# Optimization experiments

Hardware: AMD Instinct MI355X
Metric: run time of the kernel (lower is better)

Reference implementation:

```python
import jax, jax.numpy as jnp
import numpy as np

IMG = 512
STRIDES = (8.0, 16.0, 32.0)   # p3, p4, p5
ROI = 7                        # roi_size
SR = 2                         # roi_align sampling ratio (fixed; torchvision default -1 is adaptive)
IOU_LOW, IOU_HIGH = 0.4, 0.6   # fg/bg matching thresholds (2nd-stage)
NUM_CLASSES = 20
B, R, M, C = 4, 256, 40, 256


def _make_boxes(key, b, n, max_wh):
    k1, k2 = jax.random.split(key)
    cxy = jax.random.uniform(k1, (b, n, 2), minval=0.0, maxval=float(IMG))
    wh = jax.random.uniform(k2, (b, n, 2), minval=16.0, maxval=float(max_wh))
    x1y1 = jnp.clip(cxy - wh / 2, 0.0, IMG - 1.0)
    x2y2 = jnp.clip(cxy + wh / 2, x1y1 + 1.0, float(IMG))
    return jnp.concatenate([x1y1, x2y2], axis=-1)


def setup_inputs() -> dict:
    key = jax.random.key(0)
    ks = jax.random.split(key, 12)
    feats_p3 = jax.random.normal(ks[0], (B, C, 64, 64), jnp.float32)
    feats_p4 = jax.random.normal(ks[1], (B, C, 32, 32), jnp.float32)
    feats_p5 = jax.random.normal(ks[2], (B, C, 16, 16), jnp.float32)
    props_p3 = _make_boxes(ks[3], B, R, 128)
    props_p4 = _make_boxes(ks[4], B, R, 256)
    props_p5 = _make_boxes(ks[5], B, R, 512)
    gt_xyxy = _make_boxes(ks[6], B, M, 400)
    gt_cls = jax.random.randint(ks[7], (B, M, 1), 0, NUM_CLASSES).astype(jnp.float32)
    gt = jnp.concatenate([gt_xyxy, gt_cls], axis=-1)
    pad = (jnp.arange(M) >= 25)[None, :, None]   # last 15 rows are padding (class -1)
    gt_boxes = jnp.where(pad, -1.0, gt)
    conv_w = jax.random.normal(ks[8], (C, C, 3, 3), jnp.float32) * 0.01
    conv_b = jnp.zeros((C,), jnp.float32)
    fc_w = jax.random.normal(ks[9], (NUM_CLASSES + 1, C * ROI * ROI), jnp.float32) * 0.01
    fc_b = jnp.zeros((NUM_CLASSES + 1,), jnp.float32)
    return {"feats_p3": feats_p3, "feats_p4": feats_p4, "feats_p5": feats_p5,
            "props_p3": props_p3, "props_p4": props_p4, "props_p5": props_p5,
            "gt_boxes": gt_boxes, "conv_w": conv_w, "conv_b": conv_b,
            "fc_w": fc_w, "fc_b": fc_b}


def _bilinear(feat, ys, xs):
    # feat: (C,H,W); ys: (R,G,1); xs: (R,1,G) -> (C,R,G,G)
    Cc, H, W = feat.shape
    valid = (ys >= -1.0) & (ys <= H) & (xs >= -1.0) & (xs <= W)
    y = jnp.clip(ys, 0.0, H - 1.0)
    x = jnp.clip(xs, 0.0, W - 1.0)
    y0f = jnp.floor(y); x0f = jnp.floor(x)
    y0 = y0f.astype(jnp.int32); x0 = x0f.astype(jnp.int32)
    y1 = jnp.minimum(y0 + 1, H - 1); x1 = jnp.minimum(x0 + 1, W - 1)
    ly = y - y0f; lx = x - x0f
    hy = 1.0 - ly; hx = 1.0 - lx
    v = (feat[:, y0, x0] * (hy * hx) + feat[:, y0, x1] * (hy * lx)
         + feat[:, y1, x0] * (ly * hx) + feat[:, y1, x1] * (ly * lx))
    return jnp.where(valid, v, 0.0)


def _roi_align(feat, rois, scale):
    # feat: (C,H,W); rois: (R,4) xyxy in image coords; aligned=True
    r = rois.shape[0]
    x1 = rois[:, 0] * scale - 0.5
    y1 = rois[:, 1] * scale - 0.5
    roi_w = rois[:, 2] * scale - 0.5 - x1
    roi_h = rois[:, 3] * scale - 0.5 - y1
    G = ROI * SR
    frac = (jnp.arange(G, dtype=feat.dtype) + 0.5) / G
    xs = x1[:, None] + frac[None, :] * roi_w[:, None]   # (R,G)
    ys = y1[:, None] + frac[None, :] * roi_h[:, None]
    v = _bilinear(feat, ys[:, :, None], xs[:, None, :])  # (C,R,G,G)
    v = v.transpose(1, 0, 2, 3).reshape(r, -1, ROI, SR, ROI, SR)
    return v.mean(axis=(3, 5))                            # (R,C,7,7)


def _iou(b1, b2):
    # b1: (N,4), b2: (M,4) -> (N,M)
    tl = jnp.maximum(b1[:, None, :2], b2[None, :, :2])
    br = jnp.minimum(b1[:, None, 2:4], b2[None, :, 2:4])
    inter = jnp.clip(br - tl, 0.0).prod(-1)
    a1 = (b1[:, 2:4] - b1[:, :2]).prod(-1)
    a2 = (b2[:, 2:4] - b2[:, :2]).prod(-1)
    return inter / (a1[:, None] + a2[None, :] - inter)


def _match(props, gt):
    # props: (N,4); gt: (M,5) padded with class -1
    valid = gt[:, 4] != -1
    m = jnp.where(valid[None, :], _iou(props, gt[:, :4]), -1.0)
    q = m.max(axis=1)
    matched = gt[m.argmax(axis=1)]                       # (N,5)
    matched = jnp.where((q <= IOU_LOW)[:, None], -1.0, matched)      # background
    matched = jnp.where(((q > IOU_LOW) & (q < IOU_HIGH))[:, None], -1e8, matched)  # neutral
    return matched


def reference(feats_p3, feats_p4, feats_p5, props_p3, props_p4, props_p5,
              gt_boxes, conv_w, conv_b, fc_w, fc_b):
    levels = [(feats_p3, props_p3, STRIDES[0]),
              (feats_p4, props_p4, STRIDES[1]),
              (feats_p5, props_p5, STRIDES[2])]
    # ROI-align every proposal at its level; order: image-major, then level, then roi
    per_level = [jax.vmap(lambda f, p, s=s: _roi_align(f, p, 1.0 / s))(f, p)
                 for f, p, s in levels]                   # each (B,R,C,7,7)
    roi_feats = jnp.stack(per_level, axis=1).reshape(-1, C, ROI, ROI)
    # cls head: conv3x3 + relu + flatten + linear
    h = jax.lax.conv_general_dilated(roi_feats, conv_w, (1, 1), 'SAME')
    h = jax.nn.relu(h + conv_b[None, :, None, None])
    logits = h.reshape(h.shape[0], -1) @ fc_w.T + fc_b    # (B*3*R, num_classes+1)
    # match concatenated per-image proposals to GT (no-grad pipeline)
    props_all = jnp.concatenate([props_p3, props_p4, props_p5], axis=1)  # (B,3R,4)
    matched = jax.vmap(_match)(jax.lax.stop_gradient(props_all), gt_boxes)
    return logits, matched
```

## Files before the change

### kernel.cpp

```cpp
#include <hip/hip_runtime.h>

typedef unsigned short ushort_t;
typedef __attribute__((ext_vector_type(4))) unsigned short ushort4_t;
typedef __attribute__((ext_vector_type(8))) short short8;
typedef __attribute__((ext_vector_type(4))) unsigned int uint4v;
typedef __attribute__((ext_vector_type(2))) float float2v;
typedef __attribute__((ext_vector_type(4))) float floatx4;
typedef __attribute__((ext_vector_type(16))) float floatx16;

#define B_ 4
#define C_ 256
#define R_ 256
#define M_ 40
#define NCLS 21
#define ROI_ 7
#define G_ 14
#define NROI_TOT 3072
#define PROPS_PER_IMG 768
#define POOL_PITCH 264
#define POOL_ROWS 148
#define WCONV_ELEMS (256 * 2304)
#define NKB 392
#define WFC2_ELEMS (NKB * 32 * 32)
#define OFF_FWB   WCONV_ELEMS
#define OFF_CL3   (OFF_FWB + WFC2_ELEMS)
#define OFF_CL4   (OFF_CL3 + 4 * 64 * 64 * 256)
#define OFF_CL5   (OFF_CL4 + 4 * 32 * 32 * 256)

__device__ __forceinline__ ushort_t f2bf(float f) {
  unsigned u = __builtin_bit_cast(unsigned, f);
  u += 0x7fff + ((u >> 16) & 1);
  return (ushort_t)(u >> 16);
}
__device__ __forceinline__ float2v cvt2(unsigned u) {
  float2v r;
  r[0] = __builtin_bit_cast(float, u << 16);
  r[1] = __builtin_bit_cast(float, u & 0xffff0000u);
  return r;
}

template <int W>
__device__ __forceinline__ void transpose_feat(const float* __restrict__ in,
                                               ushort_t* __restrict__ outp,
                                               const int fid, const int t,
                                               ushort_t* __restrict__ tile) {
  const int b = fid / W;
  const int y = fid - b * W;
  const float* src = in + (size_t)(b * 256) * (W * W) + (size_t)y * W;
#pragma unroll
  for (int i = 0; i < W / 4; ++i) {
    const int f4 = t + i * 256;
    const int c = f4 / (W / 4);
    const int x = (f4 - c * (W / 4)) * 4;
    const floatx4 v = *(const floatx4*)(src + (size_t)c * (W * W) + x);
    tile[c * 65 + x + 0] = f2bf(v[0]);
    tile[c * 65 + x + 1] = f2bf(v[1]);
    tile[c * 65 + x + 2] = f2bf(v[2]);
    tile[c * 65 + x + 3] = f2bf(v[3]);
  }
  __syncthreads();
  ushort_t* orow = outp + ((size_t)(b * W + y) * W) * 256;
#pragma unroll
  for (int i = 0; i < W / 4; ++i) {
    const int idx = t + i * 256;
    const int x = idx >> 6;
    const int c4 = (idx & 63) * 4;
    ushort4_t v;
    v[0] = tile[(c4 + 0) * 65 + x];
    v[1] = tile[(c4 + 1) * 65 + x];
    v[2] = tile[(c4 + 2) * 65 + x];
    v[3] = tile[(c4 + 3) * 65 + x];
    *(ushort4_t*)(orow + (size_t)x * 256 + c4) = v;
  }
}

__global__ __launch_bounds__(256) void prep_kernel(
    const float* __restrict__ cw, const float* __restrict__ fw,
    const float* __restrict__ f3, const float* __restrict__ f4,
    const float* __restrict__ f5, const float* __restrict__ p3,
    const float* __restrict__ p4, const float* __restrict__ p5,
    const float* __restrict__ gt, ushort_t* __restrict__ wr,
    ushort_t* __restrict__ fwb, ushort_t* __restrict__ cl3,
    ushort_t* __restrict__ cl4, ushort_t* __restrict__ cl5,
    float* __restrict__ out) {
  __shared__ ushort_t tile[256 * 65];
  const int id = blockIdx.x;
  const int t = threadIdx.x;

  if (id < 512) {
    const int i0 = id * 256 + t;
    const int stride = 512 * 256;
    for (int idx = i0; idx < WCONV_ELEMS; idx += stride) {
      const int kk = idx >> 12;
      const int rem = idx & 4095;
      const int co = rem >> 4;
      const int i = rem & 15;
      const int k = kk * 16 + i;
      const int j = k >> 8;
      const int ci = k & 255;
      wr[idx] = f2bf(cw[(co * 256 + ci) * 9 + j]);
    }
    for (int idx = i0; idx < WFC2_ELEMS; idx += stride) {
      const int kb = idx >> 10;
      const int rem = idx & 1023;
      const int cls = rem >> 5;
      const int koff = rem & 31;
      fwb[idx] =
          (cls < NCLS) ? f2bf(fw[(size_t)cls * 12544 + kb * 32 + koff]) : 0;
    }
  } else if (id < 960) {
    const int fid = id - 512;
    if (fid < 256)      transpose_feat<64>(f3, cl3, fid, t, tile);
    else if (fid < 384) transpose_feat<32>(f4, cl4, fid - 256, t, tile);
    else                transpose_feat<16>(f5, cl5, fid - 384, t, tile);
  } else {
    const int gidx = (id - 960) * 256 + t;
    if (gidx >= NROI_TOT) return;
    const int b = gidx / PROPS_PER_IMG;
    const int i = gidx - b * PROPS_PER_IMG;
    const int lvl = i >> 8;
    const int r = i & 255;
    const float* prop =
        (lvl == 0 ? p3 : (lvl == 1 ? p4 : p5)) + (size_t)(b * R_ + r) * 4;
    const float px1 = prop[0], py1 = prop[1], px2 = prop[2], py2 = prop[3];
    const float a1 = (px2 - px1) * (py2 - py1);
    const float* gtb = gt + (size_t)b * M_ * 5;

    float best = -2.f;
    int bi = 0;
    for (int j = 0; j < M_; ++j) {
      const float gx1 = gtb[j * 5 + 0], gy1 = gtb[j * 5 + 1];
      const float gx2 = gtb[j * 5 + 2], gy2 = gtb[j * 5 + 3];
      const float cls = gtb[j * 5 + 4];
      const float tlx = fmaxf(px1, gx1), tly = fmaxf(py1, gy1);
      const float brx = fminf(px2, gx2), bry = fminf(py2, gy2);
      const float iw = fmaxf(brx - tlx, 0.f), ih = fmaxf(bry - tly, 0.f);
      const float inter = iw * ih;
      const float a2 = (gx2 - gx1) * (gy2 - gy1);
      const float iou = inter / ((a1 + a2) - inter);
      const float m = (cls != -1.0f) ? iou : -1.0f;
      if (m > best) { best = m; bi = j; }
    }
    float o0, o1, o2, o3, o4;
    if (best <= 0.4f) {
      o0 = o1 = o2 = o3 = o4 = -1.0f;
    } else if (best < 0.6f) {
      o0 = o1 = o2 = o3 = o4 = -1e8f;
    } else {
      o0 = gtb[bi * 5 + 0]; o1 = gtb[bi * 5 + 1]; o2 = gtb[bi * 5 + 2];
      o3 = gtb[bi * 5 + 3]; o4 = gtb[bi * 5 + 4];
    }
    float* od = out + (size_t)NROI_TOT * NCLS + (size_t)gidx * 5;
    od[0] = o0; od[1] = o1; od[2] = o2; od[3] = o3; od[4] = o4;
  }
}

__global__ __launch_bounds__(512, 4) void cls_head_kernel(
    const ushort_t* __restrict__ cl3, const ushort_t* __restrict__ cl4,
    const ushort_t* __restrict__ cl5, const float* __restrict__ p3,
    const float* __restrict__ p4, const float* __restrict__ p5,
    const ushort_t* __restrict__ wr, const float* __restrict__ conv_b,
    const ushort_t* __restrict__ fwb, const float* __restrict__ fc_b,
    float* __restrict__ out) {
  __shared__ __align__(16) ushort_t s_pool[POOL_ROWS * POOL_PITCH];
  __shared__ union SU {
    struct {
      int iy0[42], iy1[42], ix0[42], ix1[42];
      float ly[42], lx[42], vy[42], vx[42];
    } tb;
    float fcred[NCLS * 3 * 8];
  } s_u;

  const int bid = blockIdx.x;
  const int t = threadIdx.x;

  const int img = (bid & 7) >> 1;
  const int grp = (bid >> 3) * 2 + (bid & 1);
  const int rid0 = img * PROPS_PER_IMG + grp * 3;

  const ushort_t *clb0, *clb1, *clb2;
  const float *pr0, *pr1, *pr2;
  int W0, W1, W2;
#pragma unroll
  for (int rr = 0; rr < 3; ++rr) {
    const int rem = grp * 3 + rr;
    const int lvl = rem >> 8;
    const int r = rem & 255;
    const ushort_t* base;
    const float* pp;
    int Wl;
    if (lvl == 0) { base = cl3; pp = p3; Wl = 64; }
    else if (lvl == 1) { base = cl4; pp = p4; Wl = 32; }
    else { base = cl5; pp = p5; Wl = 16; }
    base += (size_t)img * Wl * Wl * 256;
    pp += (size_t)(img * R_ + r) * 4;
    if (rr == 0) { clb0 = base; pr0 = pp; W0 = Wl; }
    else if (rr == 1) { clb1 = base; pr1 = pp; W1 = Wl; }
    else { clb2 = base; pr2 = pp; W2 = Wl; }
  }

  if (t < POOL_PITCH) s_pool[147 * POOL_PITCH + t] = 0;

  if (t < 84) {
    const int rr = t / 28;
    const int tt = t - rr * 28;
    const float* prop = rr == 0 ? pr0 : (rr == 1 ? pr1 : pr2);
    const int H = rr == 0 ? W0 : (rr == 1 ? W1 : W2);
    const float scale = 1.0f / (float)(H == 64 ? 8 : (H == 32 ? 16 : 32));
    const float bx1 = prop[0], by1 = prop[1], bx2 = prop[2], by2 = prop[3];
    const float ax = bx1 * scale - 0.5f;
    const float ay = by1 * scale - 0.5f;
    const float rw = bx2 * scale - 0.5f - ax;
    const float rh = by2 * scale - 0.5f - ay;
    const int i = (tt < G_) ? tt : (tt - G_);
    const float frac = ((float)i + 0.5f) / (float)G_;
    const int o = rr * G_ + i;
    if (tt < G_) {
      float yy = ay + frac * rh;
      float v = (yy >= -1.0f && yy <= (float)H) ? 1.0f : 0.0f;
      float y = fminf(fmaxf(yy, 0.0f), (float)(H - 1));
      float y0f = floorf(y);
      int y0 = (int)y0f;
      s_u.tb.iy0[o] = y0;
      s_u.tb.iy1[o] = min(y0 + 1, H - 1);
      s_u.tb.ly[o] = y - y0f;
      s_u.tb.vy[o] = v;
    } else {
      float xx = ax + frac * rw;
      float v = (xx >= -1.0f && xx <= (float)H) ? 1.0f : 0.0f;
      float x = fminf(fmaxf(xx, 0.0f), (float)(H - 1));
      float x0f = floorf(x);
      int x0 = (int)x0f;
      s_u.tb.ix0[o] = x0;
      s_u.tb.ix1[o] = min(x0 + 1, H - 1);
      s_u.tb.lx[o] = x - x0f;
      s_u.tb.vx[o] = v;
    }
  }
  __syncthreads();

  const int l = t & 63;
  const int w = t >> 6;

  {
    const int hw = l >> 5;
    const int c8 = (l & 31) * 8;
    for (int cb = w * 2; cb < 147; cb += 16) {
      const int cell = cb + hw;
      if (cell >= 147) continue;
      const int rr = (cell >= 98) ? 2 : ((cell >= 49) ? 1 : 0);
      const int pos = cell - rr * 49;
      const int py = pos / 7, px = pos - (pos / 7) * 7;
      const ushort_t* clb = rr == 0 ? clb0 : (rr == 1 ? clb1 : clb2);
      const int W = rr == 0 ? W0 : (rr == 1 ? W1 : W2);
      float2v a01 = {0.f, 0.f}, a23 = {0.f, 0.f};
      float2v a45 = {0.f, 0.f}, a67 = {0.f, 0.f};
#pragma unroll
      for (int sy = 0; sy < 2; ++sy) {
        const int gy = rr * G_ + 2 * py + sy;
        const int iy0 = s_u.tb.iy0[gy], iy1 = s_u.tb.iy1[gy];
        const float ly = s_u.tb.ly[gy], vy = s_u.tb.vy[gy];
        const float hy = 1.0f - ly;
#pragma unroll
        for (int sx = 0; sx < 2; ++sx) {
          const int gx = rr * G_ + 2 * px + sx;
          const int ix0 = s_u.tb.ix0[gx], ix1 = s_u.tb.ix1[gx];
          const float lx = s_u.tb.lx[gx], vx = s_u.tb.vx[gx];
          const float hx = 1.0f - lx;
          const float vv = vy * vx;
          const float w00 = vv * hy * hx, w01 = vv * hy * lx;
          const float w10 = vv * ly * hx, w11 = vv * ly * lx;
          const uint4v u00 = *(const uint4v*)(clb + ((size_t)(iy0 * W + ix0) * 256 + c8));
          const uint4v u01 = *(const uint4v*)(clb + ((size_t)(iy0 * W + ix1) * 256 + c8));
          const uint4v u10 = *(const uint4v*)(clb + ((size_t)(iy1 * W + ix0) * 256 + c8));
          const uint4v u11 = *(const uint4v*)(clb + ((size_t)(iy1 * W + ix1) * 256 + c8));
          a01 += cvt2(u00[0]) * w00 + cvt2(u01[0]) * w01 +
                 cvt2(u10[0]) * w10 + cvt2(u11[0]) * w11;
          a23 += cvt2(u00[1]) * w00 + cvt2(u01[1]) * w01 +
                 cvt2(u10[1]) * w10 + cvt2(u11[1]) * w11;
          a45 += cvt2(u00[2]) * w00 + cvt2(u01[2]) * w01 +
                 cvt2(u10[2]) * w10 + cvt2(u11[2]) * w11;
          a67 += cvt2(u00[3]) * w00 + cvt2(u01[3]) * w01 +
                 cvt2(u10[3]) * w10 + cvt2(u11[3]) * w11;
        }
      }
      short8 pv;
      pv[0] = (short)f2bf(a01[0] * 0.25f);
      pv[1] = (short)f2bf(a01[1] * 0.25f);
      pv[2] = (short)f2bf(a23[0] * 0.25f);
      pv[3] = (short)f2bf(a23[1] * 0.25f);
      pv[4] = (short)f2bf(a45[0] * 0.25f);
      pv[5] = (short)f2bf(a45[1] * 0.25f);
      pv[6] = (short)f2bf(a67[0] * 0.25f);
      pv[7] = (short)f2bf(a67[1] * 0.25f);
      *(short8*)&s_pool[cell * POOL_PITCH + c8] = pv;
    }
  }
  __syncthreads();

  const int ml = l & 31;
  const int quad = l >> 5;
  const int co_base = w * 32;

  int gp_[5], py_[5], px_[5];
  bool ok_[5];
#pragma unroll
  for (int tt = 0; tt < 5; ++tt) {
    const int gp = tt * 32 + ml;
    gp_[tt] = gp;
    ok_[tt] = gp < 147;
    const int rr = (gp >= 98) ? 2 : ((gp >= 49) ? 1 : 0);
    const int pos = gp - rr * 49;
    py_[tt] = pos / 7;
    px_[tt] = pos - (pos / 7) * 7;
  }

  floatx16 acc[5];
#pragma unroll
  for (int a = 0; a < 5; ++a)
#pragma unroll
    for (int i = 0; i < 16; ++i) acc[a][i] = 0.f;

  const ushort_t* a0p = wr + (co_base + ml) * 16 + quad * 8;

  int kk = 0;
  for (int j = 0; j < 9; ++j) {
    const int dy = j / 3 - 1, dx = j % 3 - 1;
    int bn[5];
#pragma unroll
    for (int tt = 0; tt < 5; ++tt) {
      const int ry = py_[tt] + dy, rx = px_[tt] + dx;
      const bool okn = ok_[tt] & (ry >= 0) & (ry < 7) & (rx >= 0) & (rx < 7);
      bn[tt] = okn ? gp_[tt] + dy * 7 + dx : 147;
    }

#pragma unroll 4
    for (int kc = 0; kc < 16; ++kc, ++kk) {
      const short8 a0 = *(const short8*)(a0p + kk * 4096);
      const int cof = kc * 16 + quad * 8;
#pragma unroll
      for (int tt = 0; tt < 5; ++tt) {
        const short8 bv = *(const short8*)&s_pool[bn[tt] * POOL_PITCH + cof];
        acc[tt] =
            __builtin_amdgcn_mfma_f32_32x32x16_bf16(a0, bv, acc[tt], 0, 0, 0);
      }
    }
  }
  __syncthreads();

  ushort_t* h_lds = s_pool;
  float cbv[16];
#pragma unroll
  for (int reg = 0; reg < 16; ++reg)
    cbv[reg] = conv_b[co_base + (reg & 3) + 8 * (reg >> 2) + 4 * quad];
#pragma unroll
  for (int tt = 0; tt < 5; ++tt) {
    if (ok_[tt]) {
      const int gp = gp_[tt];
      const int rr = (gp >= 98) ? 2 : ((gp >= 49) ? 1 : 0);
      const int hbase = rr * 12544 + (gp - rr * 49);
#pragma unroll
      for (int reg = 0; reg < 16; ++reg) {
        const int co = co_base + (reg & 3) + 8 * (reg >> 2) + 4 * quad;
        h_lds[hbase + co * 49] = f2bf(fmaxf(acc[tt][reg] + cbv[reg], 0.f));
      }
    }
  }
  __syncthreads();

  {
    const int n = l & 15;
    const int kq = l >> 4;
    const ushort_t* ap0 = fwb + (n * 4 + kq) * 8;
    const ushort_t* ap1 = ap0 + 512;
    const int rb = (n < 3) ? n : 0;
    const ushort_t* bp = h_lds + (size_t)rb * 12544 + kq * 8;
    const int kb0 = w * 49;

    floatx4 fa0, fa1;
#pragma unroll
    for (int i = 0; i < 4; ++i) { fa0[i] = 0.f; fa1[i] = 0.f; }

    for (int it = 0; it < 49; ++it) {
      const int kb = kb0 + it;
      const short8 av0 = *(const short8*)(ap0 + kb * 1024);
      const short8 av1 = *(const short8*)(ap1 + kb * 1024);
      const short8 bv = *(const short8*)(bp + kb * 32);
      fa0 = __builtin_amdgcn_mfma_f32_16x16x32_bf16(av0, bv, fa0, 0, 0, 0);
      fa1 = __builtin_amdgcn_mfma_f32_16x16x32_bf16(av1, bv, fa1, 0, 0, 0);
    }
    if (n < 3) {
      const int m4 = kq * 4;
#pragma unroll
      for (int reg = 0; reg < 4; ++reg) {
        const int cls0 = m4 + reg;
        const int cls1 = 16 + m4 + reg;
        s_u.fcred[(cls0 * 3 + n) * 8 + w] = fa0[reg];
        if (cls1 < NCLS) s_u.fcred[(cls1 * 3 + n) * 8 + w] = fa1[reg];
      }
    }
  }
  __syncthreads();
  if (t < 3 * NCLS) {
    const int cls = t / 3;
    const int rr = t - cls * 3;
    const float* pr = &s_u.fcred[(cls * 3 + rr) * 8];
    float s = pr[0] + pr[1] + pr[2] + pr[3] + pr[4] + pr[5] + pr[6] + pr[7];
    out[(size_t)(rid0 + rr) * NCLS + cls] = s + fc_b[cls];
  }
}

extern "C" void kernel_launch(void* const* d_in, const int* in_sizes, int n_in,
                              void* d_out, int out_size, void* d_ws,
                              size_t ws_size, hipStream_t stream) {
  const float* f3 = (const float*)d_in[0];
  const float* f4 = (const float*)d_in[1];
  const float* f5 = (const float*)d_in[2];
  const float* p3 = (const float*)d_in[3];
  const float* p4 = (const float*)d_in[4];
  const float* p5 = (const float*)d_in[5];
  const float* gt = (const float*)d_in[6];
  const float* cw = (const float*)d_in[7];
  const float* cb = (const float*)d_in[8];
  const float* fw = (const float*)d_in[9];
  const float* fb = (const float*)d_in[10];
  float* out = (float*)d_out;

  ushort_t* wsp = (ushort_t*)d_ws;
  ushort_t* wr = wsp;
  ushort_t* fwb = wsp + OFF_FWB;
  ushort_t* cl3 = wsp + OFF_CL3;
  ushort_t* cl4 = wsp + OFF_CL4;
  ushort_t* cl5 = wsp + OFF_CL5;

  prep_kernel<<<972, 256, 0, stream>>>(cw, fw, f3, f4, f5, p3, p4, p5, gt, wr,
                                       fwb, cl3, cl4, cl5, out);
  cls_head_kernel<<<NROI_TOT / 3, 512, 0, stream>>>(cl3, cl4, cl5, p3, p4, p5,
                                                    wr, cb, fwb, fb, out);
}
```

Baseline: 319.0 us.

## Stagger second block per CU with timed sleep to desynchronize phases

Each cls_head block takes a ticket from a per-CU atomic counter, keyed by hardware CU/SE/XCC IDs. The second block to arrive on a CU sleeps for a fixed realtime tick count before starting. Co-resident blocks then run out of phase, so one block's memory-bound ROI gather overlaps another's compute-bound MFMA work. The cost is a deliberate delay, an atomic per block, and counters that prep_kernel must zero, with behaviour tied to the hardware-ID register layout.

```diff
diff --git a/kernel.cpp b/kernel.cpp
--- a/kernel.cpp
+++ b/kernel.cpp
@@ -26,6 +26,9 @@
 #define OFF_CL3   (OFF_FWB + WFC2_ELEMS)
 #define OFF_CL4   (OFF_CL3 + 4 * 64 * 64 * 256)
 #define OFF_CL5   (OFF_CL4 + 4 * 32 * 32 * 256)
+#define OFF_CTR   (OFF_CL5 + 4 * 16 * 16 * 256)
+#define NCTR 1024
+#define STAG_TICKS 1800ull
 
 __device__ __forceinline__ ushort_t f2bf(float f) {
   unsigned u = __builtin_bit_cast(unsigned, f);
@@ -82,12 +85,15 @@
     const float* __restrict__ gt, ushort_t* __restrict__ wr,
     ushort_t* __restrict__ fwb, ushort_t* __restrict__ cl3,
     ushort_t* __restrict__ cl4, ushort_t* __restrict__ cl5,
-    float* __restrict__ out) {
+    unsigned* __restrict__ ctr, float* __restrict__ out) {
   __shared__ ushort_t tile[256 * 65];
   const int id = blockIdx.x;
   const int t = threadIdx.x;
 
   if (id < 512) {
+    if (id == 0) {
+      ctr[t] = 0; ctr[t + 256] = 0; ctr[t + 512] = 0; ctr[t + 768] = 0;
+    }
     const int i0 = id * 256 + t;
     const int stride = 512 * 256;
     for (int idx = i0; idx < WCONV_ELEMS; idx += stride) {
@@ -161,7 +167,7 @@
     const float* __restrict__ p4, const float* __restrict__ p5,
     const ushort_t* __restrict__ wr, const float* __restrict__ conv_b,
     const ushort_t* __restrict__ fwb, const float* __restrict__ fc_b,
-    float* __restrict__ out) {
+    unsigned* __restrict__ ctr, float* __restrict__ out) {
   __shared__ __align__(16) ushort_t s_pool[POOL_ROWS * POOL_PITCH];
   __shared__ union SU {
     struct {
@@ -170,9 +176,26 @@
     } tb;
     float fcred[NCLS * 3 * 8];
   } s_u;
+  __shared__ unsigned s_ticket;
 
   const int bid = blockIdx.x;
   const int t = threadIdx.x;
+
+  if (t == 0) {
+    unsigned hwid = 0, xcc = 0;
+    asm volatile("s_getreg_b32 %0, hwreg(HW_REG_HW_ID)" : "=s"(hwid));
+    asm volatile("s_getreg_b32 %0, hwreg(HW_REG_XCC_ID)" : "=s"(xcc));
+    const unsigned cu = (hwid >> 8) & 15;
+    const unsigned se = (hwid >> 13) & 7;
+    const unsigned idx = (((xcc & 7) * 8 + se) * 16 + cu) & (NCTR - 1);
+    s_ticket = atomicAdd(&ctr[idx], 1u);
+  }
+  __syncthreads();
+  if (s_ticket == 1) {
+    const unsigned long long t0 = __builtin_amdgcn_s_memrealtime();
+    while (__builtin_amdgcn_s_memrealtime() - t0 < STAG_TICKS)
+      __builtin_amdgcn_s_sleep(64);
+  }
 
   const int img = (bid & 7) >> 1;
   const int grp = (bid >> 3) * 2 + (bid & 1);
@@ -432,9 +455,10 @@
   ushort_t* cl3 = wsp + OFF_CL3;
   ushort_t* cl4 = wsp + OFF_CL4;
   ushort_t* cl5 = wsp + OFF_CL5;
+  unsigned* ctr = (unsigned*)(wsp + OFF_CTR);
 
   prep_kernel<<<972, 256, 0, stream>>>(cw, fw, f3, f4, f5, p3, p4, p5, gt, wr,
-                                       fwb, cl3, cl4, cl5, out);
+                                       fwb, cl3, cl4, cl5, ctr, out);
   cls_head_kernel<<<NROI_TOT / 3, 512, 0, stream>>>(cl3, cl4, cl5, p3, p4, p5,
-                                                    wr, cb, fwb, fb, out);
-}
+                                                    wr, cb, fwb, fb, ctr, out);
+}
```

Result: slower. 326.9 us (+2.5%).
